# Kernel optimization log

Hardware: AMD Instinct MI355X
Metric: run time of the kernel (lower is better)

Reference implementation:

```python
import jax, jax.numpy as jnp
import numpy as np

D, B, V = 8, 4096, 1024          # token fields (type..section), batch streams, vocab per field
THRES = 0.9                      # top_k filter_thres default
TEMP = 1.0                       # temperature default
NOTE_TYPE = 1                    # note_type_code; sos=0, eos=2


def setup_inputs() -> dict:
    key = jax.random.key(0)
    k1, k2, k3 = jax.random.split(key, 3)
    logits = jax.random.normal(k1, (D, B, V), dtype=jnp.float32)
    u = jax.random.uniform(k2, (D, B, V), dtype=jnp.float32)
    current_values = jax.random.randint(k3, (D, B), 0, 16).astype(jnp.int32)
    return {"logits": logits, "u": u, "current_values": current_values}


def reference(logits, u, current_values):
    neg = -jnp.inf
    ar = jnp.arange(V)
    # monotonicity mask: positions < current value are forbidden  [D,B,V]
    lg = jnp.where(ar[None, None, :] < current_values[:, :, None], neg, logits)
    # index 0 is masked for every field (logits[d][:, 0] = -inf in the loop)
    lg = lg.at[:, :, 0].set(neg)
    # top-k filtering: keep values >= k-th largest, k = int((1 - thres) * V)
    k = int((1.0 - THRES) * V)
    kth = jax.lax.top_k(lg, k)[0][..., -1:]          # [D,B,1]
    filt = jnp.where(lg < kth, neg, lg)
    logp = jax.nn.log_softmax(filt / TEMP, axis=-1)  # stable softmax, -inf -> prob 0
    probs = jnp.exp(logp)
    # multinomial sampling via Gumbel-max using provided uniform noise
    eps = 1e-20
    gumbel = -jnp.log(-jnp.log(u + eps) + eps)
    samples = jnp.argmax(logp + gumbel, axis=-1)     # [D,B]
    # type-conditional fill: fields 1..7 are zero unless sampled type == NOTE
    is_note = samples[0] == NOTE_TYPE                # [B]
    keep = (jnp.arange(D)[:, None] == 0) | is_note[None, :]
    tokens = jnp.where(keep, samples, 0)             # [D,B]
    return tokens.T, probs                           # [B,D] int, [D,B,V] float
```

## Files before the change

### kernel.cpp

```cpp
#include <hip/hip_runtime.h>
#include <math.h>

#define DD 8
#define BB 4096
#define VV 1024
#define K_SEL 102
#define RPB 4
#define TOPBITS 16

__device__ __forceinline__ unsigned f2key(float f) {
    unsigned u = __float_as_uint(f);
    unsigned m = (unsigned)((int)u >> 31) | 0x80000000u;
    return u ^ m;
}
__device__ __forceinline__ float key2f(unsigned k) {
    unsigned m = 0x80000000u | ~((unsigned)((int)k >> 31));
    return __uint_as_float(k ^ m);
}

__global__ __launch_bounds__(256) void decode_row_kernel(
    const float* __restrict__ logits,
    const float* __restrict__ unoise,
    const int* __restrict__ curvals,
    float* __restrict__ probs_out,
    int* __restrict__ samples)
{
    const int wave = threadIdx.x >> 6;
    const int lane = threadIdx.x & 63;
    const int row  = blockIdx.x * RPB + wave;

    const float4* l4 = (const float4*)(logits + (size_t)row * VV);
    const float4* u4 = (const float4*)(unoise + (size_t)row * VV);
    const int cv1 = max(curvals[row], 1);

    unsigned key[16];
#pragma unroll
    for (int i = 0; i < 4; i++) {
        float4 ff = l4[i * 64 + lane];
        const int vb = i * 256 + lane * 4;
        float e[4] = {ff.x, ff.y, ff.z, ff.w};
#pragma unroll
        for (int j = 0; j < 4; j++) {
            float t = (vb + j < cv1) ? -INFINITY : e[j];
            key[i * 4 + j] = f2key(t);
        }
    }

    unsigned p  = 0u;
    unsigned kk = K_SEL;
#pragma unroll
    for (int b = 31; b >= 32 - TOPBITS; --b) {
        const unsigned tgt = (p >> b) | 1u;
        unsigned n = 0;
#pragma unroll
        for (int i = 0; i < 16; i++)
            n += (unsigned)__popcll(__ballot((key[i] >> b) == tgt));
        if (n >= kk) p |= (1u << b);
        else         kk -= n;
    }

    const unsigned PMASK = ~((1u << (32 - TOPBITS)) - 1u);
    unsigned cmask = 0u;
#pragma unroll
    for (int i = 0; i < 16; i++)
        if ((key[i] & PMASK) == p) cmask |= (1u << i);
    unsigned thr;
    for (;;) {
        unsigned mx = 0u;
#pragma unroll
        for (int i = 0; i < 16; i++)
            if (cmask & (1u << i)) mx = max(mx, key[i]);
#pragma unroll
        for (int off = 32; off; off >>= 1)
            mx = max(mx, (unsigned)__shfl_xor((int)mx, off, 64));
        if (kk <= 1u) { thr = mx; break; }
        unsigned ceq = 0u;
#pragma unroll
        for (int i = 0; i < 16; i++)
            ceq += (unsigned)__popcll(__ballot(key[i] == mx));
        if (kk <= ceq) { thr = mx; break; }
        kk -= ceq;
#pragma unroll
        for (int i = 0; i < 16; i++)
            if (key[i] == mx) cmask &= ~(1u << i);
    }

    unsigned mk = key[0];
#pragma unroll
    for (int i = 1; i < 16; i++) mk = max(mk, key[i]);
#pragma unroll
    for (int off = 32; off; off >>= 1)
        mk = max(mk, (unsigned)__shfl_xor((int)mk, off, 64));
    const float m = key2f(mk);

    float ex[16];
    float s = 0.0f;
#pragma unroll
    for (int i = 0; i < 16; i++) {
        float e = (key[i] >= thr) ? __expf(key2f(key[i]) - m) : 0.0f;
        ex[i] = e;
        s += e;
    }
    float4 uu[4];
#pragma unroll
    for (int i = 0; i < 4; i++) uu[i] = u4[i * 64 + lane];
#pragma unroll
    for (int off = 32; off; off >>= 1)
        s += __shfl_xor(s, off, 64);
    const float inv = 1.0f / s;

    float bnum = 0.0f, bden = 1.0f;
    int   besti = VV;
    float4* p4 = (float4*)(probs_out + (size_t)row * VV);
#pragma unroll
    for (int i = 0; i < 4; i++) {
        float4 pv;
        pv.x = ex[i * 4 + 0] * inv;
        pv.y = ex[i * 4 + 1] * inv;
        pv.z = ex[i * 4 + 2] * inv;
        pv.w = ex[i * 4 + 3] * inv;
        p4[i * 64 + lane] = pv;
        float us[4] = {uu[i].x, uu[i].y, uu[i].z, uu[i].w};
#pragma unroll
        for (int j = 0; j < 4; j++) {
            const int idx = i * 4 + j;
            float nl = 1e-20f - __logf(us[j] + 1e-20f);
            float a  = ex[idx];
            int v = i * 256 + lane * 4 + j;
            if (a * bden > bnum * nl) { bnum = a; bden = nl; besti = v; }
        }
    }
#pragma unroll
    for (int off = 32; off; off >>= 1) {
        float onum = __shfl_xor(bnum, off, 64);
        float oden = __shfl_xor(bden, off, 64);
        int   oi   = __shfl_xor(besti, off, 64);
        float x = onum * bden, y = bnum * oden;
        if (x > y || (x == y && oi < besti)) { bnum = onum; bden = oden; besti = oi; }
    }
    if (lane == 0) samples[row] = besti;
}

__global__ __launch_bounds__(256) void tokens_kernel(
    const int* __restrict__ samples, float* __restrict__ tokens_out)
{
    int i = blockIdx.x * 256 + threadIdx.x;
    int b = i >> 3;
    int d = i & 7;
    int sm = samples[d * BB + b];
    int t0 = samples[b];
    tokens_out[i] = (d == 0 || t0 == 1) ? (float)sm : 0.0f;
}

extern "C" void kernel_launch(void* const* d_in, const int* in_sizes, int n_in,
                              void* d_out, int out_size, void* d_ws, size_t ws_size,
                              hipStream_t stream) {
    const float* logits = (const float*)d_in[0];
    const float* unoise = (const float*)d_in[1];
    const int*   curvals = (const int*)d_in[2];

    float* out        = (float*)d_out;
    float* tokens_out = out;
    float* probs_out  = out + (size_t)BB * DD;
    int*   samples    = (int*)d_ws;

    decode_row_kernel<<<(DD * BB) / RPB, 256, 0, stream>>>(logits, unoise, curvals,
                                                           probs_out, samples);
    tokens_kernel<<<(BB * DD) / 256, 256, 0, stream>>>(samples, tokens_out);
}
```

Before: 318.4 us.

## Prefetch noise early, radix-4 threshold search, nontemporal loads/stores, occupancy hint

The uniform-noise load now issues at kernel start together with the logits loads, so its latency overlaps the threshold search. The radix select that finds the top-k threshold now resolves two bits per step instead of one, which halves the number of sequential steps but triples the ballots per step. Noise loads and probability stores use nontemporal hints to limit cache pollution, and launch bounds request 8 blocks per CU. Keeping the noise live from the start adds 16 registers per thread, which could work against the occupancy target.

Result: no change. 316.4 us (-0.6%).

```diff
diff --git a/kernel.cpp b/kernel.cpp
--- a/kernel.cpp
+++ b/kernel.cpp
@@ -7,6 +7,8 @@
 #define K_SEL 102
 #define RPB 4
 #define TOPBITS 16
+
+typedef float vf4 __attribute__((ext_vector_type(4)));
 
 __device__ __forceinline__ unsigned f2key(float f) {
     unsigned u = __float_as_uint(f);
@@ -18,7 +20,7 @@
     return __uint_as_float(k ^ m);
 }
 
-__global__ __launch_bounds__(256) void decode_row_kernel(
+__global__ __launch_bounds__(256, 8) void decode_row_kernel(
     const float* __restrict__ logits,
     const float* __restrict__ unoise,
     const int* __restrict__ curvals,
@@ -29,19 +31,24 @@
     const int lane = threadIdx.x & 63;
     const int row  = blockIdx.x * RPB + wave;
 
-    const float4* l4 = (const float4*)(logits + (size_t)row * VV);
-    const float4* u4 = (const float4*)(unoise + (size_t)row * VV);
+    const vf4* l4 = (const vf4*)(logits + (size_t)row * VV);
+    const vf4* u4 = (const vf4*)(unoise + (size_t)row * VV);
     const int cv1 = max(curvals[row], 1);
+
+    vf4 lf[4];
+#pragma unroll
+    for (int i = 0; i < 4; i++) lf[i] = l4[i * 64 + lane];
+    vf4 uu[4];
+#pragma unroll
+    for (int i = 0; i < 4; i++) uu[i] = __builtin_nontemporal_load(&u4[i * 64 + lane]);
 
     unsigned key[16];
 #pragma unroll
     for (int i = 0; i < 4; i++) {
-        float4 ff = l4[i * 64 + lane];
         const int vb = i * 256 + lane * 4;
-        float e[4] = {ff.x, ff.y, ff.z, ff.w};
 #pragma unroll
         for (int j = 0; j < 4; j++) {
-            float t = (vb + j < cv1) ? -INFINITY : e[j];
+            float t = (vb + j < cv1) ? -INFINITY : lf[i][j];
             key[i * 4 + j] = f2key(t);
         }
     }
@@ -49,14 +56,21 @@
     unsigned p  = 0u;
     unsigned kk = K_SEL;
 #pragma unroll
-    for (int b = 31; b >= 32 - TOPBITS; --b) {
-        const unsigned tgt = (p >> b) | 1u;
-        unsigned n = 0;
+    for (int b = 30; b >= 32 - TOPBITS; b -= 2) {
+        const unsigned pb = p >> b;
+        unsigned n3 = 0, n2 = 0, n1 = 0;
 #pragma unroll
-        for (int i = 0; i < 16; i++)
-            n += (unsigned)__popcll(__ballot((key[i] >> b) == tgt));
-        if (n >= kk) p |= (1u << b);
-        else         kk -= n;
+        for (int i = 0; i < 16; i++) {
+            unsigned t = key[i] >> b;
+            n3 += (unsigned)__popcll(__ballot(t == (pb | 3u)));
+            n2 += (unsigned)__popcll(__ballot(t == (pb | 2u)));
+            n1 += (unsigned)__popcll(__ballot(t == (pb | 1u)));
+        }
+        const unsigned c3 = n3, c2 = n3 + n2, c1 = n3 + n2 + n1;
+        if (kk <= c3)      { p |= 3u << b; }
+        else if (kk <= c2) { p |= 2u << b; kk -= c3; }
+        else if (kk <= c1) { p |= 1u << b; kk -= c2; }
+        else               {               kk -= c1; }
     }
 
     const unsigned PMASK = ~((1u << (32 - TOPBITS)) - 1u);
@@ -101,9 +115,6 @@
         ex[i] = e;
         s += e;
     }
-    float4 uu[4];
-#pragma unroll
-    for (int i = 0; i < 4; i++) uu[i] = u4[i * 64 + lane];
 #pragma unroll
     for (int off = 32; off; off >>= 1)
         s += __shfl_xor(s, off, 64);
@@ -111,20 +122,19 @@
 
     float bnum = 0.0f, bden = 1.0f;
     int   besti = VV;
-    float4* p4 = (float4*)(probs_out + (size_t)row * VV);
+    vf4* p4 = (vf4*)(probs_out + (size_t)row * VV);
 #pragma unroll
     for (int i = 0; i < 4; i++) {
-        float4 pv;
+        vf4 pv;
         pv.x = ex[i * 4 + 0] * inv;
         pv.y = ex[i * 4 + 1] * inv;
         pv.z = ex[i * 4 + 2] * inv;
         pv.w = ex[i * 4 + 3] * inv;
-        p4[i * 64 + lane] = pv;
-        float us[4] = {uu[i].x, uu[i].y, uu[i].z, uu[i].w};
+        __builtin_nontemporal_store(pv, &p4[i * 64 + lane]);
 #pragma unroll
         for (int j = 0; j < 4; j++) {
             const int idx = i * 4 + j;
-            float nl = 1e-20f - __logf(us[j] + 1e-20f);
+            float nl = 1e-20f - __logf(uu[i][j] + 1e-20f);
             float a  = ex[idx];
             int v = i * 256 + lane * 4 + j;
             if (a * bden > bnum * nl) { bnum = a; bden = nl; besti = v; }
```
